# Kernel optimization log

Measured on AMD Instinct MI355X. Metric: run time of the kernel, lower is better.

## Reference

```python
import jax, jax.numpy as jnp
import numpy as np

# TT structure: W is [in_features, out_features] = [4096, 4096]
IN_FACTORS = (16, 16, 16)
OUT_FACTORS = (16, 16, 16)
RANKS = (1, 8, 8, 1)
BATCH = 8192
IN_FEATURES = 4096
OUT_FEATURES = 4096
ITER_NUM = 3
L = 1.0
S = -1.0
EPSILON = 1.0


def tt_dense_matmul(cores, mat):
    """Multiply TT-matrix (cores[k]: [r_{k-1}, m_k, n_k, r_k]) by dense mat [prod(n), P].
    Returns [prod(m), P]. Sequential core contractions, never materializes dense W."""
    P = mat.shape[1]
    data = mat.reshape(1, mat.shape[0], P)  # [r=1, N_rem, T]
    M = 1
    for core in cores:
        r0, m, n, r1 = core.shape
        nrem = data.shape[1]
        d4 = data.reshape(r0, n, nrem // n, -1)            # [r0, n_k, N_rem', T]
        data = jnp.einsum('rmns,rnat->satm', core, d4)      # [r1, N_rem', T, m_k]
        data = data.reshape(r1, nrem // n, -1)              # fold m_k into trailing T
        M *= m
    return data.reshape(P, M).T  # [M, P]


def tt_tt_mul(cores_a, cores_b):
    """TT-matrix product: cores of A [M,K] and B [K,N] -> cores of A@B with Kronecker ranks."""
    out = []
    for ca, cb in zip(cores_a, cores_b):
        a0, m, n, a1 = ca.shape
        b0, n2, l, b1 = cb.shape
        c = jnp.einsum('amnb,cnld->acmlbd', ca, cb)
        out.append(c.reshape(a0 * b0, m, l, a1 * b1))
    return out


def setup_inputs() -> dict:
    key = jax.random.key(0)
    ks = jax.random.split(key, 5)
    x = jax.random.normal(ks[0], (BATCH, IN_FEATURES), dtype=jnp.float32)
    # TT cores of weight W [in, out]: core_k shape [r_{k-1}, in_k, out_k, r_k]
    core_std = 0.3  # glorot-like per-core scale
    cores = []
    for k in range(3):
        shp = (RANKS[k], IN_FACTORS[k], OUT_FACTORS[k], RANKS[k + 1])
        cores.append(core_std * jax.random.normal(ks[k + 1], shp, dtype=jnp.float32))
    bias = 0.01 * jnp.ones((OUT_FEATURES,), dtype=jnp.float32)
    return {"x": x, "core0": cores[0], "core1": cores[1], "core2": cores[2], "bias": bias}


def reference(x, core0, core1, core2, bias):
    cores = [core0, core1, core2]
    # weight_t = t3.transpose(weight): swap in/out mode of each core
    cores_t = [c.transpose(0, 2, 1, 3) for c in cores]  # W^T: [out, in]
    x_t = x.T  # [in, B]
    mv = tt_dense_matmul(cores_t, x_t).T  # x @ W, [B, out]
    # norm-gated shrinkage init
    norm_x = jnp.linalg.norm(x)
    x_l = (mv + bias) / L + jnp.where(norm_x > EPSILON, 0.0, S)
    # G = W^T @ W in TT form (ranks grow to 64)
    G = tt_tt_mul(cores_t, cores)
    for _ in range(1, ITER_NUM):
        nrm = jnp.linalg.norm(x_l)
        term = tt_dense_matmul(G, x_l.T).T  # x_l @ (W^T W), [B, out]
        x_l = x_l - term / L + mv / L + bias + jnp.where(nrm > EPSILON, 0.0, S)
    return x_l
```

## Files before the change

kernel.cpp:

```cpp
#include <hip/hip_runtime.h>
#include <stdint.h>

typedef __bf16 bf16;
typedef __bf16 bf16x4 __attribute__((ext_vector_type(4)));
typedef __bf16 bf16x8 __attribute__((ext_vector_type(8)));
typedef float f32x4 __attribute__((ext_vector_type(4)));

#define GLD_LDS16(g, l)                                                        \
  __builtin_amdgcn_global_load_lds(                                            \
      (const __attribute__((address_space(1))) void*)(g),                      \
      (__attribute__((address_space(3))) void*)(l), 16, 0, 0)

#define BAR() asm volatile("s_barrier" ::: "memory")
#define VMW(n) asm volatile("s_waitcnt vmcnt(" #n ")" ::: "memory")
#define PRIO(x) __builtin_amdgcn_s_setprio(x)

__global__ void k_init(float* s) {
  if (threadIdx.x < 3) s[threadIdx.x] = 0.0f;
}

__global__ __launch_bounds__(256) void k_pre(
    const float* __restrict__ x, const float* __restrict__ c0,
    const float* __restrict__ c1, const float* __restrict__ c2,
    bf16* __restrict__ Wt, bf16* __restrict__ xb, float* __restrict__ ssq,
    float* __restrict__ g0, float* __restrict__ g1, float* __restrict__ g2) {
  const int b = blockIdx.x;
  if (b < 4096) {
    const int j = b;
    const int j0 = j >> 8, j1 = (j >> 4) & 15, j2 = j & 15;
    const int t = threadIdx.x;
    const int i0 = t >> 4, i1 = t & 15;
    float t0[8];
    {
      float4 v0 = *(const float4*)&c0[(i0 * 16 + j0) * 8];
      float4 v1 = *(const float4*)&c0[(i0 * 16 + j0) * 8 + 4];
      t0[0] = v0.x; t0[1] = v0.y; t0[2] = v0.z; t0[3] = v0.w;
      t0[4] = v1.x; t0[5] = v1.y; t0[6] = v1.z; t0[7] = v1.w;
    }
    float a[8];
#pragma unroll
    for (int r2 = 0; r2 < 8; ++r2) a[r2] = 0.f;
#pragma unroll
    for (int r1 = 0; r1 < 8; ++r1) {
      const float* row = &c1[((r1 * 16 + i1) * 16 + j1) * 8];
      float4 u0 = *(const float4*)row;
      float4 u1 = *(const float4*)(row + 4);
      a[0] += t0[r1] * u0.x; a[1] += t0[r1] * u0.y;
      a[2] += t0[r1] * u0.z; a[3] += t0[r1] * u0.w;
      a[4] += t0[r1] * u1.x; a[5] += t0[r1] * u1.y;
      a[6] += t0[r1] * u1.z; a[7] += t0[r1] * u1.w;
    }
    union { bf16 h[16]; bf16x8 v[2]; } u;
#pragma unroll
    for (int i2 = 0; i2 < 16; ++i2) {
      float s = 0.f;
#pragma unroll
      for (int r2 = 0; r2 < 8; ++r2) s += a[r2] * c2[(r2 * 16 + i2) * 16 + j2];
      u.h[i2] = (bf16)s;
    }
    bf16* dst = Wt + (size_t)j * 4096 + i0 * 256 + i1 * 16;
    ((bf16x8*)dst)[0] = u.v[0];
    ((bf16x8*)dst)[1] = u.v[1];
  } else if (b < 5120) {
    const int n4 = 8192 * 4096 / 4;
    int tid = (b - 4096) * 256 + threadIdx.x;
    const int stride = 1024 * 256;
    const float4* x4 = (const float4*)x;
    bf16x4* xb4 = (bf16x4*)xb;
    float acc = 0.f;
    for (int i = tid; i < n4; i += stride) {
      float4 v = x4[i];
      acc += v.x * v.x + v.y * v.y + v.z * v.z + v.w * v.w;
      bf16x4 bb;
      bb.x = (bf16)v.x; bb.y = (bf16)v.y; bb.z = (bf16)v.z; bb.w = (bf16)v.w;
      xb4[i] = bb;
    }
#pragma unroll
    for (int off = 32; off; off >>= 1) acc += __shfl_down(acc, off);
    __shared__ float red[4];
    if ((threadIdx.x & 63) == 0) red[threadIdx.x >> 6] = acc;
    __syncthreads();
    if (threadIdx.x == 0) atomicAdd(ssq, red[0] + red[1] + red[2] + red[3]);
  } else {
    int tid = (b - 5120) * 256 + threadIdx.x;
    if (tid < 16384) {
      int jj = tid >> 6, p1 = tid & 63;
      int j0 = jj >> 4, j0p = jj & 15, r1 = p1 >> 3, r1p = p1 & 7;
      float s = 0.f;
#pragma unroll
      for (int i0 = 0; i0 < 16; ++i0)
        s += c0[(i0 * 16 + j0) * 8 + r1] * c0[(i0 * 16 + j0p) * 8 + r1p];
      g0[tid] = s;
    } else if (tid < 32768) {
      int k = tid - 16384;
      int p2 = k >> 8, jj = k & 255;
      int r2 = p2 >> 3, r2p = p2 & 7, j2 = jj >> 4, j2p = jj & 15;
      float s = 0.f;
#pragma unroll
      for (int i2 = 0; i2 < 16; ++i2)
        s += c2[(r2 * 16 + i2) * 16 + j2] * c2[(r2p * 16 + i2) * 16 + j2p];
      g2[k] = s;
    } else {
      int k = tid - 32768;
      int p2 = k & 63, rest = k >> 6;
      int j1p = rest & 15, j1 = (rest >> 4) & 15, p1 = rest >> 8;
      int r1 = p1 >> 3, r1p = p1 & 7, r2 = p2 >> 3, r2p = p2 & 7;
      float s = 0.f;
#pragma unroll
      for (int i1 = 0; i1 < 16; ++i1)
        s += c1[((r1 * 16 + i1) * 16 + j1) * 8 + r2] *
             c1[((r1p * 16 + i1) * 16 + j1p) * 8 + r2p];
      g1[k] = s;
    }
  }
}

__global__ __launch_bounds__(256) void k_buildG(const float* __restrict__ g0,
                                                const float* __restrict__ g1,
                                                const float* __restrict__ g2,
                                                bf16* __restrict__ G) {
  __shared__ float s_g2[16384];
  __shared__ float s_g1[4096];
  __shared__ float s_g0m[16384];
  const int t = threadIdx.x;
  const int j1 = blockIdx.x >> 4, j1p = blockIdx.x & 15;
  const int jj1 = j1 * 16 + j1p;

  const float4* g2f4 = (const float4*)g2;
  float4* sg2f4 = (float4*)s_g2;
  for (int k = t; k < 4096; k += 256) sg2f4[k] = g2f4[k];
  const float4* g1f4 = (const float4*)g1;
  float4* sg1f4 = (float4*)s_g1;
  for (int k = t; k < 1024; k += 256) {
    int p1 = k >> 4, q = k & 15;
    sg1f4[k] = g1f4[(p1 * 256 + jj1) * 16 + q];
  }
#pragma unroll
  for (int q = 0; q < 16; ++q) {
    float4 v = ((const float4*)g0)[t * 16 + q];
    s_g0m[(q * 4 + 0) * 256 + t] = v.x;
    s_g0m[(q * 4 + 1) * 256 + t] = v.y;
    s_g0m[(q * 4 + 2) * 256 + t] = v.z;
    s_g0m[(q * 4 + 3) * 256 + t] = v.w;
  }
  __syncthreads();

  float m[64];
#pragma unroll
  for (int i = 0; i < 64; ++i) m[i] = 0.f;
#pragma unroll 4
  for (int p1 = 0; p1 < 64; ++p1) {
    float av = s_g0m[p1 * 256 + t];
#pragma unroll
    for (int q = 0; q < 16; ++q) {
      float4 v = ((const float4*)s_g1)[p1 * 16 + q];
      m[q * 4 + 0] += av * v.x; m[q * 4 + 1] += av * v.y;
      m[q * 4 + 2] += av * v.z; m[q * 4 + 3] += av * v.w;
    }
  }
  __syncthreads();
#pragma unroll
  for (int p2 = 0; p2 < 64; ++p2) s_g0m[p2 * 256 + t] = m[p2];
  __syncthreads();

  const int bcol = (t & 15) * 16;
  const int j2 = t & 15;
#pragma unroll 1
  for (int rep = 0; rep < 2; ++rep) {
    const int r0 = (((t >> 4) + rep * 16)) * 8;
    float acc2[8][16];
#pragma unroll
    for (int i = 0; i < 8; ++i)
#pragma unroll
      for (int c = 0; c < 16; ++c) acc2[i][c] = 0.f;
#pragma unroll 2
    for (int p2 = 0; p2 < 64; ++p2) {
      float4 mv0 = *(const float4*)&s_g0m[p2 * 256 + r0];
      float4 mv1 = *(const float4*)&s_g0m[p2 * 256 + r0 + 4];
      float mv[8] = {mv0.x, mv0.y, mv0.z, mv0.w, mv1.x, mv1.y, mv1.z, mv1.w};
      float gv[16];
#pragma unroll
      for (int q = 0; q < 4; ++q) {
        float4 v = *(const float4*)&s_g2[p2 * 256 + bcol + q * 4];
        gv[q * 4 + 0] = v.x; gv[q * 4 + 1] = v.y;
        gv[q * 4 + 2] = v.z; gv[q * 4 + 3] = v.w;
      }
#pragma unroll
      for (int i = 0; i < 8; ++i)
#pragma unroll
        for (int c = 0; c < 16; ++c) acc2[i][c] += mv[i] * gv[c];
    }
#pragma unroll
    for (int i = 0; i < 8; ++i) {
      const int jj0 = r0 + i;
      const int j0 = jj0 >> 4, j0p = jj0 & 15;
      bf16* d = G + (size_t)(j0 * 256 + j1 * 16 + j2) * 4096 + (j0p * 256 + j1p * 16);
      union { bf16 h[16]; bf16x8 v[2]; } u;
#pragma unroll
      for (int c = 0; c < 16; ++c) u.h[c] = (bf16)acc2[i][c];
      ((bf16x8*)d)[0] = u.v[0];
      ((bf16x8*)d)[1] = u.v[1];
    }
  }
}

#define STAGE_A(h, kt, b)                                                              \
  do {                                                                                 \
    GLD_LDS16(srcA + (size_t)((h) * 128) * K + (kt) * 64,                              \
              smem + (b) * 65536 + (h) * 16384 + wofs);                                \
    GLD_LDS16(srcA + (size_t)((h) * 128 + 64) * K + (kt) * 64,                         \
              smem + (b) * 65536 + (h) * 16384 + 8192 + wofs);                         \
  } while (0)
#define STAGE_B(h, kt, b)                                                              \
  do {                                                                                 \
    GLD_LDS16(srcB + (size_t)((h) * 128) * K + (kt) * 64,                              \
              smem + (b) * 65536 + 32768 + (h) * 16384 + wofs);                        \
    GLD_LDS16(srcB + (size_t)((h) * 128 + 64) * K + (kt) * 64,                         \
              smem + (b) * 65536 + 32768 + (h) * 16384 + 8192 + wofs);                 \
  } while (0)
#define LDA(ms, b)                                                                     \
  do {                                                                                 \
    const char* s_ = smem + (b) * 65536 + (ms) * 16384 + aRow;                         \
    _Pragma("unroll") for (int mi_ = 0; mi_ < 4; ++mi_) {                              \
      af[mi_][0] = *(const bf16x8*)(s_ + mi_ * 2048 + cb0);                            \
      af[mi_][1] = *(const bf16x8*)(s_ + mi_ * 2048 + cb1);                            \
    }                                                                                  \
  } while (0)
#define LDB(ns, b)                                                                     \
  do {                                                                                 \
    const char* s_ = smem + (b) * 65536 + 32768 + (ns) * 16384 + bRow;                 \
    _Pragma("unroll") for (int ni_ = 0; ni_ < 2; ++ni_) {                              \
      bfr[ns][ni_][0] = *(const bf16x8*)(s_ + ni_ * 2048 + cb0);                       \
      bfr[ns][ni_][1] = *(const bf16x8*)(s_ + ni_ * 2048 + cb1);                       \
    }                                                                                  \
  } while (0)
#define MQ(ms, ns)                                                                     \
  do {                                                                                 \
    PRIO(1);                                                                           \
    _Pragma("unroll") for (int mi_ = 0; mi_ < 4; ++mi_)                                \
    _Pragma("unroll") for (int ni_ = 0; ni_ < 2; ++ni_)                                \
    _Pragma("unroll") for (int ks_ = 0; ks_ < 2; ++ks_)                                \
        acc[(ms) * 4 + mi_][(ns) * 2 + ni_] =                                          \
            __builtin_amdgcn_mfma_f32_16x16x32_bf16(                                   \
                af[mi_][ks_], bfr[ns][ni_][ks_],                                       \
                acc[(ms) * 4 + mi_][(ns) * 2 + ni_], 0, 0, 0);                         \
    PRIO(0);                                                                           \
  } while (0)

__device__ __forceinline__ void run_core(const bf16* __restrict__ Ag,
                                         const bf16* __restrict__ Bg, const int K,
                                         const int bx, const int by, char* smem,
                                         f32x4 (&acc)[8][4]) {
  const int t = threadIdx.x;
  const int w = t >> 6, lane = t & 63;
  const int q = lane >> 4, lr = lane & 15;
  const int wm = w & 1, wn = w >> 1;

  const int r0 = t >> 3;
  const int ksrc = (t & 7) ^ (r0 & 7);
  const bf16* srcA = Ag + (size_t)(by * 256 + r0) * K + ksrc * 8;
  const bf16* srcB = Bg + (size_t)(bx * 256 + r0) * K + ksrc * 8;
  const int wofs = w << 10;

  const int aRow = (wm * 64 + lr) * 128;
  const int bRow = (wn * 32 + lr) * 128;
  const int cb0 = ((q ^ (lr & 7)) << 4);
  const int cb1 = (((4 + q) ^ (lr & 7)) << 4);

#pragma unroll
  for (int i = 0; i < 8; ++i)
#pragma unroll
    for (int j = 0; j < 4; ++j) acc[i][j] = (f32x4){0.f, 0.f, 0.f, 0.f};

  bf16x8 af[4][2];
  bf16x8 bfr[2][2][2];

  STAGE_A(0, 0, 0); STAGE_B(0, 0, 0); STAGE_B(1, 0, 0); STAGE_A(1, 0, 0);
  STAGE_A(0, 1, 1); STAGE_B(0, 1, 1); STAGE_B(1, 1, 1);
  VMW(6);
  BAR();

  const int NT = K >> 6;
#pragma unroll 1
  for (int tt = 0; tt + 3 < NT; tt += 2) {
    STAGE_A(1, tt + 1, 1);
    LDB(0, 0); LDA(0, 0); LDB(1, 0);
    MQ(0, 0); MQ(0, 1);
    BAR();
    STAGE_A(0, tt + 2, 0); STAGE_B(0, tt + 2, 0); STAGE_B(1, tt + 2, 0);
    LDA(1, 0);
    MQ(1, 1); MQ(1, 0);
    VMW(6);
    BAR();
    STAGE_A(1, tt + 2, 0);
    LDB(0, 1); LDA(0, 1); LDB(1, 1);
    MQ(0, 0); MQ(0, 1);
    BAR();
    STAGE_A(0, tt + 3, 1); STAGE_B(0, tt + 3, 1); STAGE_B(1, tt + 3, 1);
    LDA(1, 1);
    MQ(1, 1); MQ(1, 0);
    VMW(6);
    BAR();
  }

  STAGE_A(1, NT - 1, 1);
  LDB(0, 0); LDA(0, 0); LDB(1, 0);
  MQ(0, 0); MQ(0, 1);
  BAR();
  LDA(1, 0);
  MQ(1, 1); MQ(1, 0);
  VMW(0);
  BAR();
  LDB(0, 1); LDA(0, 1); LDB(1, 1);
  MQ(0, 0); MQ(0, 1);
  BAR();
  LDA(1, 1);
  MQ(1, 1); MQ(1, 0);
}

template <int MODE>
__global__ __launch_bounds__(512, 2) void k_gemm(
    const bf16* __restrict__ A, const bf16* __restrict__ Bt, int M, int N, int K,
    const float* __restrict__ bias, const bf16* __restrict__ xl0,
    const bf16* __restrict__ xl_prev, float* f32_out, bf16* __restrict__ bf_out,
    const float* __restrict__ ssq_a, const float* __restrict__ ssq_b,
    float* __restrict__ ssq_out) {
  const int nb = gridDim.x * gridDim.y;
  const int lin = blockIdx.y * gridDim.x + blockIdx.x;
  const int sw = (lin & 7) * (nb >> 3) + (lin >> 3);
  const int bx = sw % gridDim.x, by = sw / gridDim.x;
  __shared__ char smem[131072];

  float gate = 0.f;
  if constexpr (MODE == 0) {
    gate = (*ssq_a > 1.0f) ? 0.f : -1.f;
  } else {
    float g0v = (*ssq_a > 1.0f) ? 0.f : -1.f;
    float gtv = (*ssq_b > 1.0f) ? 0.f : -1.f;
    gate = gtv - g0v;
  }
  VMW(0);

  f32x4 acc[8][4];
  run_core(A, Bt, K, bx, by, smem, acc);

  const int t = threadIdx.x;
  const int w = t >> 6, lane = t & 63;
  const int q = lane >> 4, lr = lane & 15;
  const int wm = w & 1, wn = w >> 1;
  float ssql = 0.f;
#pragma unroll
  for (int mi = 0; mi < 8; ++mi) {
    const int grow = by * 256 + ((mi & 4) ? 128 : 0) + wm * 64 + (mi & 3) * 16 + q * 4;
#pragma unroll
    for (int r = 0; r < 4; ++r) {
      const size_t rowb = (size_t)(grow + r) * N;
#pragma unroll
      for (int ni = 0; ni < 4; ++ni) {
        const int gcol = bx * 256 + ((ni & 2) ? 128 : 0) + wn * 32 + (ni & 1) * 16 + lr;
        const size_t idx = rowb + gcol;
        float v = acc[mi][ni][r];
        if constexpr (MODE == 0) {
          float xl = v + bias[gcol] + gate;
          bf_out[idx] = (bf16)xl;
          ssql += xl * xl;
        } else if constexpr (MODE == 2) {
          float xl = 2.0f * (float)xl0[idx] - v + gate;
          bf_out[idx] = (bf16)xl;
          ssql += xl * xl;
        } else {
          f32_out[idx] = (float)xl_prev[idx] - v + (float)xl0[idx] + gate;
        }
      }
    }
  }
  if constexpr (MODE == 0 || MODE == 2) {
#pragma unroll
    for (int off = 32; off; off >>= 1) ssql += __shfl_down(ssql, off);
    __syncthreads();
    float* red = (float*)smem;
    if (lane == 0) red[w] = ssql;
    __syncthreads();
    if (t == 0) {
      float s = 0.f;
#pragma unroll
      for (int i = 0; i < 8; ++i) s += red[i];
      atomicAdd(ssq_out, s);
    }
  }
}

extern "C" void kernel_launch(void* const* d_in, const int* in_sizes, int n_in,
                              void* d_out, int out_size, void* d_ws, size_t ws_size,
                              hipStream_t stream) {
  const float* x = (const float*)d_in[0];
  const float* c0 = (const float*)d_in[1];
  const float* c1 = (const float*)d_in[2];
  const float* c2 = (const float*)d_in[3];
  const float* bias = (const float*)d_in[4];
  float* out = (float*)d_out;

  const int B = 8192, F = 4096;
  char* ws = (char*)d_ws;
  float* scal = (float*)ws;
  bf16* xbf = (bf16*)(ws + 256);
  bf16* Wt = (bf16*)(ws + 256 + (size_t)67108864);
  bf16* G = (bf16*)(ws + 256 + (size_t)100663296);
  bf16* xl0 = (bf16*)(ws + 256 + (size_t)134217728);
  bf16* xl1 = xbf;
  float* g0 = (float*)xl0;
  float* g2 = g0 + 16384;
  float* g1 = g2 + 16384;

  k_init<<<1, 64, 0, stream>>>(scal);
  k_pre<<<9344, 256, 0, stream>>>(x, c0, c1, c2, Wt, xbf, &scal[0], g0, g1, g2);
  k_buildG<<<256, 256, 0, stream>>>(g0, g1, g2, G);

  dim3 g1d(F / 256, B / 256);
  k_gemm<0><<<g1d, 512, 0, stream>>>(xbf, Wt, B, F, F, bias, nullptr, nullptr,
                                     nullptr, xl0, &scal[0], nullptr, &scal[1]);
  k_gemm<2><<<g1d, 512, 0, stream>>>(xl0, G, B, F, F, nullptr, xl0, nullptr,
                                     nullptr, xl1, &scal[0], &scal[1], &scal[2]);
  k_gemm<3><<<g1d, 512, 0, stream>>>(xl1, G, B, F, F, nullptr, xl0, xl1,
                                     out, nullptr, &scal[0], &scal[2], nullptr);
}
```

Baseline: 974.4 us.

## Switch GEMM to 32x32x16 MFMA and replace init kernel with deterministic partial-sum reduction

The GEMM inner loop now uses 32x32x16 bf16 MFMA instructions with 32-row fragments instead of 16x16x32, which changes the LDS fragment loads, accumulator layout and epilogue indexing. The larger MFMA shape cuts the number of instructions and LDS reads per FLOP. Separately, the k_init launch and the per-block atomicAdd for the input norm are removed: k_pre writes per-block partial sums and block 0 of k_buildG reduces them and zeroes the other scalars. That saves one launch and the atomics, at the cost of a serial reduction inside buildG.

```diff
diff --git a/kernel.cpp b/kernel.cpp
--- a/kernel.cpp
+++ b/kernel.cpp
@@ -5,6 +5,7 @@
 typedef __bf16 bf16x4 __attribute__((ext_vector_type(4)));
 typedef __bf16 bf16x8 __attribute__((ext_vector_type(8)));
 typedef float f32x4 __attribute__((ext_vector_type(4)));
+typedef float f32x16 __attribute__((ext_vector_type(16)));
 
 #define GLD_LDS16(g, l)                                                        \
   __builtin_amdgcn_global_load_lds(                                            \
@@ -15,14 +16,10 @@
 #define VMW(n) asm volatile("s_waitcnt vmcnt(" #n ")" ::: "memory")
 #define PRIO(x) __builtin_amdgcn_s_setprio(x)
 
-__global__ void k_init(float* s) {
-  if (threadIdx.x < 3) s[threadIdx.x] = 0.0f;
-}
-
 __global__ __launch_bounds__(256) void k_pre(
     const float* __restrict__ x, const float* __restrict__ c0,
     const float* __restrict__ c1, const float* __restrict__ c2,
-    bf16* __restrict__ Wt, bf16* __restrict__ xb, float* __restrict__ ssq,
+    bf16* __restrict__ Wt, bf16* __restrict__ xb, float* __restrict__ pbuf,
     float* __restrict__ g0, float* __restrict__ g1, float* __restrict__ g2) {
   const int b = blockIdx.x;
   if (b < 4096) {
@@ -80,7 +77,7 @@
     __shared__ float red[4];
     if ((threadIdx.x & 63) == 0) red[threadIdx.x >> 6] = acc;
     __syncthreads();
-    if (threadIdx.x == 0) atomicAdd(ssq, red[0] + red[1] + red[2] + red[3]);
+    if (threadIdx.x == 0) pbuf[b - 4096] = red[0] + red[1] + red[2] + red[3];
   } else {
     int tid = (b - 5120) * 256 + threadIdx.x;
     if (tid < 16384) {
@@ -118,11 +115,27 @@
 __global__ __launch_bounds__(256) void k_buildG(const float* __restrict__ g0,
                                                 const float* __restrict__ g1,
                                                 const float* __restrict__ g2,
-                                                bf16* __restrict__ G) {
+                                                bf16* __restrict__ G,
+                                                const float* __restrict__ pbuf,
+                                                float* __restrict__ scal) {
   __shared__ float s_g2[16384];
   __shared__ float s_g1[4096];
   __shared__ float s_g0m[16384];
   const int t = threadIdx.x;
+
+  if (blockIdx.x == 0) {
+    float a = pbuf[t * 4] + pbuf[t * 4 + 1] + pbuf[t * 4 + 2] + pbuf[t * 4 + 3];
+#pragma unroll
+    for (int off = 32; off; off >>= 1) a += __shfl_down(a, off);
+    if ((t & 63) == 0) s_g1[t >> 6] = a;
+    __syncthreads();
+    if (t == 0) {
+      scal[0] = s_g1[0] + s_g1[1] + s_g1[2] + s_g1[3];
+      scal[1] = 0.f; scal[2] = 0.f;
+    }
+    __syncthreads();
+  }
+
   const int j1 = blockIdx.x >> 4, j1p = blockIdx.x & 15;
   const int jj1 = j1 * 16 + j1p;
 
@@ -218,43 +231,41 @@
     GLD_LDS16(srcB + (size_t)((h) * 128 + 64) * K + (kt) * 64,                         \
               smem + (b) * 65536 + 32768 + (h) * 16384 + 8192 + wofs);                 \
   } while (0)
-#define LDA(ms, b)                                                                     \
+#define LDA_H(h, b)                                                                    \
   do {                                                                                 \
-    const char* s_ = smem + (b) * 65536 + (ms) * 16384 + aRow;                         \
-    _Pragma("unroll") for (int mi_ = 0; mi_ < 4; ++mi_) {                              \
-      af[mi_][0] = *(const bf16x8*)(s_ + mi_ * 2048 + cb0);                            \
-      af[mi_][1] = *(const bf16x8*)(s_ + mi_ * 2048 + cb1);                            \
-    }                                                                                  \
+    const char* s_ = smem + (b) * 65536 + (h) * 16384 + aBase;                         \
+    _Pragma("unroll") for (int mL_ = 0; mL_ < 2; ++mL_)                                \
+    _Pragma("unroll") for (int ks_ = 0; ks_ < 4; ++ks_)                                \
+        af[mL_][ks_] = *(const bf16x8*)(s_ + mL_ * 4096 +                              \
+                                        (((ks_ * 2 + hi) ^ l7) << 4));                 \
   } while (0)
-#define LDB(ns, b)                                                                     \
+#define LDB_ALL(b)                                                                     \
   do {                                                                                 \
-    const char* s_ = smem + (b) * 65536 + 32768 + (ns) * 16384 + bRow;                 \
-    _Pragma("unroll") for (int ni_ = 0; ni_ < 2; ++ni_) {                              \
-      bfr[ns][ni_][0] = *(const bf16x8*)(s_ + ni_ * 2048 + cb0);                       \
-      bfr[ns][ni_][1] = *(const bf16x8*)(s_ + ni_ * 2048 + cb1);                       \
-    }                                                                                  \
+    const char* s_ = smem + (b) * 65536 + 32768 + bBase;                               \
+    _Pragma("unroll") for (int ni_ = 0; ni_ < 2; ++ni_)                                \
+    _Pragma("unroll") for (int ks_ = 0; ks_ < 4; ++ks_)                                \
+        bfr[ni_][ks_] = *(const bf16x8*)(s_ + ni_ * 16384 +                            \
+                                         (((ks_ * 2 + hi) ^ l7) << 4));                \
   } while (0)
-#define MQ(ms, ns)                                                                     \
+#define MQ_H(h)                                                                        \
   do {                                                                                 \
     PRIO(1);                                                                           \
-    _Pragma("unroll") for (int mi_ = 0; mi_ < 4; ++mi_)                                \
+    _Pragma("unroll") for (int ks_ = 0; ks_ < 4; ++ks_)                                \
+    _Pragma("unroll") for (int mL_ = 0; mL_ < 2; ++mL_)                                \
     _Pragma("unroll") for (int ni_ = 0; ni_ < 2; ++ni_)                                \
-    _Pragma("unroll") for (int ks_ = 0; ks_ < 2; ++ks_)                                \
-        acc[(ms) * 4 + mi_][(ns) * 2 + ni_] =                                          \
-            __builtin_amdgcn_mfma_f32_16x16x32_bf16(                                   \
-                af[mi_][ks_], bfr[ns][ni_][ks_],                                       \
-                acc[(ms) * 4 + mi_][(ns) * 2 + ni_], 0, 0, 0);                         \
+        acc[(h) * 2 + mL_][ni_] = __builtin_amdgcn_mfma_f32_32x32x16_bf16(             \
+            af[mL_][ks_], bfr[ni_][ks_], acc[(h) * 2 + mL_][ni_], 0, 0, 0);            \
     PRIO(0);                                                                           \
   } while (0)
 
 __device__ __forceinline__ void run_core(const bf16* __restrict__ Ag,
                                          const bf16* __restrict__ Bg, const int K,
                                          const int bx, const int by, char* smem,
-                                         f32x4 (&acc)[8][4]) {
+                                         f32x16 (&acc)[4][2]) {
   const int t = threadIdx.x;
   const int w = t >> 6, lane = t & 63;
-  const int q = lane >> 4, lr = lane & 15;
   const int wm = w & 1, wn = w >> 1;
+  const int lr32 = lane & 31, hi = lane >> 5, l7 = lane & 7;
 
   const int r0 = t >> 3;
   const int ksrc = (t & 7) ^ (r0 & 7);
@@ -262,18 +273,16 @@
   const bf16* srcB = Bg + (size_t)(bx * 256 + r0) * K + ksrc * 8;
   const int wofs = w << 10;
 
-  const int aRow = (wm * 64 + lr) * 128;
-  const int bRow = (wn * 32 + lr) * 128;
-  const int cb0 = ((q ^ (lr & 7)) << 4);
-  const int cb1 = (((4 + q) ^ (lr & 7)) << 4);
-
-#pragma unroll
-  for (int i = 0; i < 8; ++i)
-#pragma unroll
-    for (int j = 0; j < 4; ++j) acc[i][j] = (f32x4){0.f, 0.f, 0.f, 0.f};
-
-  bf16x8 af[4][2];
-  bf16x8 bfr[2][2][2];
+  const int aBase = (wm * 64 + lr32) * 128;
+  const int bBase = (wn * 32 + lr32) * 128;
+
+#pragma unroll
+  for (int i = 0; i < 4; ++i)
+#pragma unroll
+    for (int j = 0; j < 2; ++j) acc[i][j] = (f32x16)(0.f);
+
+  bf16x8 af[2][4];
+  bf16x8 bfr[2][4];
 
   STAGE_A(0, 0, 0); STAGE_B(0, 0, 0); STAGE_B(1, 0, 0); STAGE_A(1, 0, 0);
   STAGE_A(0, 1, 1); STAGE_B(0, 1, 1); STAGE_B(1, 1, 1);
@@ -284,38 +293,38 @@
 #pragma unroll 1
   for (int tt = 0; tt + 3 < NT; tt += 2) {
     STAGE_A(1, tt + 1, 1);
-    LDB(0, 0); LDA(0, 0); LDB(1, 0);
-    MQ(0, 0); MQ(0, 1);
+    LDB_ALL(0); LDA_H(0, 0);
+    MQ_H(0);
     BAR();
     STAGE_A(0, tt + 2, 0); STAGE_B(0, tt + 2, 0); STAGE_B(1, tt + 2, 0);
-    LDA(1, 0);
-    MQ(1, 1); MQ(1, 0);
+    LDA_H(1, 0);
+    MQ_H(1);
     VMW(6);
     BAR();
     STAGE_A(1, tt + 2, 0);
-    LDB(0, 1); LDA(0, 1); LDB(1, 1);
-    MQ(0, 0); MQ(0, 1);
+    LDB_ALL(1); LDA_H(0, 1);
+    MQ_H(0);
     BAR();
     STAGE_A(0, tt + 3, 1); STAGE_B(0, tt + 3, 1); STAGE_B(1, tt + 3, 1);
-    LDA(1, 1);
-    MQ(1, 1); MQ(1, 0);
+    LDA_H(1, 1);
+    MQ_H(1);
     VMW(6);
     BAR();
   }
 
   STAGE_A(1, NT - 1, 1);
-  LDB(0, 0); LDA(0, 0); LDB(1, 0);
-  MQ(0, 0); MQ(0, 1);
+  LDB_ALL(0); LDA_H(0, 0);
+  MQ_H(0);
   BAR();
-  LDA(1, 0);
-  MQ(1, 1); MQ(1, 0);
+  LDA_H(1, 0);
+  MQ_H(1);
   VMW(0);
   BAR();
-  LDB(0, 1); LDA(0, 1); LDB(1, 1);
-  MQ(0, 0); MQ(0, 1);
+  LDB_ALL(1); LDA_H(0, 1);
+  MQ_H(0);
   BAR();
-  LDA(1, 1);
-  MQ(1, 1); MQ(1, 0);
+  LDA_H(1, 1);
+  MQ_H(1);
 }
 
 template <int MODE>
@@ -341,27 +350,29 @@
   }
   VMW(0);
 
-  f32x4 acc[8][4];
+  f32x16 acc[4][2];
   run_core(A, Bt, K, bx, by, smem, acc);
 
   const int t = threadIdx.x;
   const int w = t >> 6, lane = t & 63;
-  const int q = lane >> 4, lr = lane & 15;
   const int wm = w & 1, wn = w >> 1;
+  const int lr32 = lane & 31, hi = lane >> 5;
   float ssql = 0.f;
 #pragma unroll
-  for (int mi = 0; mi < 8; ++mi) {
-    const int grow = by * 256 + ((mi & 4) ? 128 : 0) + wm * 64 + (mi & 3) * 16 + q * 4;
-#pragma unroll
-    for (int r = 0; r < 4; ++r) {
-      const size_t rowb = (size_t)(grow + r) * N;
-#pragma unroll
-      for (int ni = 0; ni < 4; ++ni) {
-        const int gcol = bx * 256 + ((ni & 2) ? 128 : 0) + wn * 32 + (ni & 1) * 16 + lr;
-        const size_t idx = rowb + gcol;
-        float v = acc[mi][ni][r];
+  for (int mi = 0; mi < 4; ++mi) {
+    const int rowB = by * 256 + (mi >> 1) * 128 + wm * 64 + (mi & 1) * 32 + hi * 4;
+#pragma unroll
+    for (int ni = 0; ni < 2; ++ni) {
+      const int gcol = bx * 256 + ni * 128 + wn * 32 + lr32;
+      float bs = 0.f;
+      if constexpr (MODE == 0) bs = bias[gcol];
+#pragma unroll
+      for (int rg = 0; rg < 16; ++rg) {
+        const int row = rowB + (rg & 3) + 8 * (rg >> 2);
+        const size_t idx = (size_t)row * N + gcol;
+        float v = acc[mi][ni][rg];
         if constexpr (MODE == 0) {
-          float xl = v + bias[gcol] + gate;
+          float xl = v + bs + gate;
           bf_out[idx] = (bf16)xl;
           ssql += xl * xl;
         } else if constexpr (MODE == 2) {
@@ -411,10 +422,10 @@
   float* g0 = (float*)xl0;
   float* g2 = g0 + 16384;
   float* g1 = g2 + 16384;
-
-  k_init<<<1, 64, 0, stream>>>(scal);
-  k_pre<<<9344, 256, 0, stream>>>(x, c0, c1, c2, Wt, xbf, &scal[0], g0, g1, g2);
-  k_buildG<<<256, 256, 0, stream>>>(g0, g1, g2, G);
+  float* pbuf = g1 + 1048576;
+
+  k_pre<<<9344, 256, 0, stream>>>(x, c0, c1, c2, Wt, xbf, pbuf, g0, g1, g2);
+  k_buildG<<<256, 256, 0, stream>>>(g0, g1, g2, G, pbuf, scal);
 
   dim3 g1d(F / 256, B / 256);
   k_gemm<0><<<g1d, 512, 0, stream>>>(xbf, Wt, B, F, F, bias, nullptr, nullptr,
```

Result: slower. 1.076 ms (+10.5%).

## Fold Gram-core computation and norm reduction into buildG, drop init kernel

Applied to the files above, without the earlier changes.

Removes the k_init launch and the g0/g1/g2 Gram-core blocks from k_pre. k_buildG now computes those small Gram contractions itself, redundantly in each of its 256 blocks, from core data staged in shared memory. The squared norm of x is now written as per-block partial sums to a buffer and reduced deterministically by block 0 of buildG, which also zeroes the other scalars, replacing the atomicAdd. This saves a launch and a global round-trip for the small tensors, at the cost of repeated per-block compute and higher register pressure in buildG.

```diff
diff --git a/kernel.cpp b/kernel.cpp
--- a/kernel.cpp
+++ b/kernel.cpp
@@ -15,15 +15,10 @@
 #define VMW(n) asm volatile("s_waitcnt vmcnt(" #n ")" ::: "memory")
 #define PRIO(x) __builtin_amdgcn_s_setprio(x)
 
-__global__ void k_init(float* s) {
-  if (threadIdx.x < 3) s[threadIdx.x] = 0.0f;
-}
-
 __global__ __launch_bounds__(256) void k_pre(
     const float* __restrict__ x, const float* __restrict__ c0,
     const float* __restrict__ c1, const float* __restrict__ c2,
-    bf16* __restrict__ Wt, bf16* __restrict__ xb, float* __restrict__ ssq,
-    float* __restrict__ g0, float* __restrict__ g1, float* __restrict__ g2) {
+    bf16* __restrict__ Wt, bf16* __restrict__ xb, float* __restrict__ pbuf) {
   const int b = blockIdx.x;
   if (b < 4096) {
     const int j = b;
@@ -61,7 +56,7 @@
     bf16* dst = Wt + (size_t)j * 4096 + i0 * 256 + i1 * 16;
     ((bf16x8*)dst)[0] = u.v[0];
     ((bf16x8*)dst)[1] = u.v[1];
-  } else if (b < 5120) {
+  } else {
     const int n4 = 8192 * 4096 / 4;
     int tid = (b - 4096) * 256 + threadIdx.x;
     const int stride = 1024 * 256;
@@ -80,69 +75,110 @@
     __shared__ float red[4];
     if ((threadIdx.x & 63) == 0) red[threadIdx.x >> 6] = acc;
     __syncthreads();
-    if (threadIdx.x == 0) atomicAdd(ssq, red[0] + red[1] + red[2] + red[3]);
-  } else {
-    int tid = (b - 5120) * 256 + threadIdx.x;
-    if (tid < 16384) {
-      int jj = tid >> 6, p1 = tid & 63;
-      int j0 = jj >> 4, j0p = jj & 15, r1 = p1 >> 3, r1p = p1 & 7;
-      float s = 0.f;
-#pragma unroll
-      for (int i0 = 0; i0 < 16; ++i0)
-        s += c0[(i0 * 16 + j0) * 8 + r1] * c0[(i0 * 16 + j0p) * 8 + r1p];
-      g0[tid] = s;
-    } else if (tid < 32768) {
-      int k = tid - 16384;
-      int p2 = k >> 8, jj = k & 255;
-      int r2 = p2 >> 3, r2p = p2 & 7, j2 = jj >> 4, j2p = jj & 15;
-      float s = 0.f;
-#pragma unroll
-      for (int i2 = 0; i2 < 16; ++i2)
-        s += c2[(r2 * 16 + i2) * 16 + j2] * c2[(r2p * 16 + i2) * 16 + j2p];
-      g2[k] = s;
-    } else {
-      int k = tid - 32768;
-      int p2 = k & 63, rest = k >> 6;
-      int j1p = rest & 15, j1 = (rest >> 4) & 15, p1 = rest >> 8;
-      int r1 = p1 >> 3, r1p = p1 & 7, r2 = p2 >> 3, r2p = p2 & 7;
-      float s = 0.f;
-#pragma unroll
-      for (int i1 = 0; i1 < 16; ++i1)
-        s += c1[((r1 * 16 + i1) * 16 + j1) * 8 + r2] *
-             c1[((r1p * 16 + i1) * 16 + j1p) * 8 + r2p];
-      g1[k] = s;
-    }
+    if (threadIdx.x == 0) pbuf[b - 4096] = red[0] + red[1] + red[2] + red[3];
   }
 }
 
-__global__ __launch_bounds__(256) void k_buildG(const float* __restrict__ g0,
-                                                const float* __restrict__ g1,
-                                                const float* __restrict__ g2,
-                                                bf16* __restrict__ G) {
+__global__ __launch_bounds__(256) void k_buildG(const float* __restrict__ c0,
+                                                const float* __restrict__ c1,
+                                                const float* __restrict__ c2,
+                                                bf16* __restrict__ G,
+                                                const float* __restrict__ pbuf,
+                                                float* __restrict__ scal) {
   __shared__ float s_g2[16384];
-  __shared__ float s_g1[4096];
   __shared__ float s_g0m[16384];
+  __shared__ float s_cc[4096];
   const int t = threadIdx.x;
   const int j1 = blockIdx.x >> 4, j1p = blockIdx.x & 15;
-  const int jj1 = j1 * 16 + j1p;
-
-  const float4* g2f4 = (const float4*)g2;
-  float4* sg2f4 = (float4*)s_g2;
-  for (int k = t; k < 4096; k += 256) sg2f4[k] = g2f4[k];
-  const float4* g1f4 = (const float4*)g1;
-  float4* sg1f4 = (float4*)s_g1;
-  for (int k = t; k < 1024; k += 256) {
-    int p1 = k >> 4, q = k & 15;
-    sg1f4[k] = g1f4[(p1 * 256 + jj1) * 16 + q];
-  }
-#pragma unroll
-  for (int q = 0; q < 16; ++q) {
-    float4 v = ((const float4*)g0)[t * 16 + q];
-    s_g0m[(q * 4 + 0) * 256 + t] = v.x;
-    s_g0m[(q * 4 + 1) * 256 + t] = v.y;
-    s_g0m[(q * 4 + 2) * 256 + t] = v.z;
-    s_g0m[(q * 4 + 3) * 256 + t] = v.w;
-  }
+
+  if (blockIdx.x == 0) {
+    float a = pbuf[t * 4] + pbuf[t * 4 + 1] + pbuf[t * 4 + 2] + pbuf[t * 4 + 3];
+#pragma unroll
+    for (int off = 32; off; off >>= 1) a += __shfl_down(a, off);
+    if ((t & 63) == 0) s_g2[t >> 6] = a;
+    __syncthreads();
+    if (t == 0) {
+      scal[0] = s_g2[0] + s_g2[1] + s_g2[2] + s_g2[3];
+      scal[1] = 0.f; scal[2] = 0.f;
+    }
+    __syncthreads();
+  }
+
+  {
+    const float4* c0f = (const float4*)c0;
+    const float4* c2f = (const float4*)c2;
+    const float4* c1f = (const float4*)c1;
+    float4* cc = (float4*)s_cc;
+    float4* cm = (float4*)s_g0m;
+    for (int k = t; k < 512; k += 256) cc[k] = c0f[k];
+    for (int k = t; k < 512; k += 256) cc[512 + k] = c2f[k];
+    for (int k = t; k < 4096; k += 256) cm[k] = c1f[k];
+  }
+  __syncthreads();
+
+  {
+    float accg[64];
+#pragma unroll
+    for (int i = 0; i < 64; ++i) accg[i] = 0.f;
+    const int j2 = t >> 4, j2p = t & 15;
+    const float* c2L = s_cc + 2048;
+#pragma unroll 1
+    for (int i2 = 0; i2 < 16; ++i2) {
+      float a2[8], b2[8];
+#pragma unroll
+      for (int r = 0; r < 8; ++r) {
+        a2[r] = c2L[(r * 16 + i2) * 16 + j2];
+        b2[r] = c2L[(r * 16 + i2) * 16 + j2p];
+      }
+#pragma unroll
+      for (int p2 = 0; p2 < 64; ++p2) accg[p2] += a2[p2 >> 3] * b2[p2 & 7];
+    }
+#pragma unroll
+    for (int p2 = 0; p2 < 64; ++p2) s_g2[p2 * 256 + t] = accg[p2];
+  }
+
+  float g0acc[64];
+  {
+#pragma unroll
+    for (int i = 0; i < 64; ++i) g0acc[i] = 0.f;
+    const int j0 = t >> 4, j0p = t & 15;
+#pragma unroll 1
+    for (int i0 = 0; i0 < 16; ++i0) {
+      float a0[8], b0[8];
+#pragma unroll
+      for (int r = 0; r < 8; ++r) {
+        a0[r] = s_cc[(i0 * 16 + j0) * 8 + r];
+        b0[r] = s_cc[(i0 * 16 + j0p) * 8 + r];
+      }
+#pragma unroll
+      for (int p1 = 0; p1 < 64; ++p1) g0acc[p1] += a0[p1 >> 3] * b0[p1 & 7];
+    }
+  }
+  float g1acc[16];
+  {
+#pragma unroll
+    for (int i = 0; i < 16; ++i) g1acc[i] = 0.f;
+    const int p1 = t >> 2, r1 = p1 >> 3, r1p = p1 & 7;
+#pragma unroll 1
+    for (int i1 = 0; i1 < 16; ++i1) {
+      float a1[8], b1[8];
+#pragma unroll
+      for (int r = 0; r < 8; ++r) {
+        a1[r] = s_g0m[((r1 * 16 + i1) * 16 + j1) * 8 + r];
+        b1[r] = s_g0m[((r1p * 16 + i1) * 16 + j1p) * 8 + r];
+      }
+#pragma unroll
+      for (int v = 0; v < 16; ++v) {
+        int p2 = (t & 3) * 16 + v;
+        g1acc[v] += a1[p2 >> 3] * b1[p2 & 7];
+      }
+    }
+  }
+  __syncthreads();
+#pragma unroll
+  for (int p1 = 0; p1 < 64; ++p1) s_g0m[p1 * 256 + t] = g0acc[p1];
+#pragma unroll
+  for (int v = 0; v < 16; ++v) s_cc[(t >> 2) * 64 + (t & 3) * 16 + v] = g1acc[v];
   __syncthreads();
 
   float m[64];
@@ -153,7 +189,7 @@
     float av = s_g0m[p1 * 256 + t];
 #pragma unroll
     for (int q = 0; q < 16; ++q) {
-      float4 v = ((const float4*)s_g1)[p1 * 16 + q];
+      float4 v = ((const float4*)s_cc)[p1 * 16 + q];
       m[q * 4 + 0] += av * v.x; m[q * 4 + 1] += av * v.y;
       m[q * 4 + 2] += av * v.z; m[q * 4 + 3] += av * v.w;
     }
@@ -408,13 +444,10 @@
   bf16* G = (bf16*)(ws + 256 + (size_t)100663296);
   bf16* xl0 = (bf16*)(ws + 256 + (size_t)134217728);
   bf16* xl1 = xbf;
-  float* g0 = (float*)xl0;
-  float* g2 = g0 + 16384;
-  float* g1 = g2 + 16384;
-
-  k_init<<<1, 64, 0, stream>>>(scal);
-  k_pre<<<9344, 256, 0, stream>>>(x, c0, c1, c2, Wt, xbf, &scal[0], g0, g1, g2);
-  k_buildG<<<256, 256, 0, stream>>>(g0, g1, g2, G);
+  float* pbuf = (float*)xl0;
+
+  k_pre<<<5120, 256, 0, stream>>>(x, c0, c1, c2, Wt, xbf, pbuf);
+  k_buildG<<<256, 256, 0, stream>>>(c0, c1, c2, G, pbuf, scal);
 
   dim3 g1d(F / 256, B / 256);
   k_gemm<0><<<g1d, 512, 0, stream>>>(xbf, Wt, B, F, F, bias, nullptr, nullptr,
```

After: 993.7 us. About the same (+2.0%).
